# Kernel tuning notes

Hardware: AMD Instinct MI355X
Metric: run time of the kernel (lower is better)

The kernel has to match this reference:

```python
import jax, jax.numpy as jnp
import numpy as np

N_NODES = 50000
K_NEIGH = 32
D_IN = 128
D_OUT = 128
LEAKY_ALPHA = 0.2  # tf.nn.leaky_relu default


def setup_inputs() -> dict:
    key = jax.random.key(0)
    k1, k2, k3, k4 = jax.random.split(key, 4)
    glorot = lambda k, shape: jax.random.uniform(
        k, shape, jnp.float32, -1.0, 1.0) * np.sqrt(6.0 / (shape[0] + shape[1]))
    return {
        "self_vecs": jax.random.normal(k1, (N_NODES, D_IN), jnp.float32),
        "neigh_vecs": jax.random.normal(k2, (N_NODES * K_NEIGH, D_IN), jnp.float32),
        "feat_weights": glorot(k3, (D_IN, D_OUT)),
        "attn_weights": glorot(k4, (D_OUT, 1)),
        "bias": jnp.zeros((D_OUT,), jnp.float32),
        "num_neighbors": K_NEIGH,
    }


def reference(self_vecs, neigh_vecs, feat_weights, attn_weights, bias, num_neighbors):
    n = self_vecs.shape[0]
    from_neighs = neigh_vecs @ feat_weights            # [N*K, Dout]
    h_self = self_vecs @ feat_weights                  # [N, Dout]
    neigh_logits = (from_neighs @ attn_weights).reshape(n, num_neighbors)  # [N, K]
    self_logits = h_self @ attn_weights                # [N, 1]
    logits = neigh_logits + self_logits                # [N, K]
    coefs = jax.nn.softmax(jax.nn.leaky_relu(logits, LEAKY_ALPHA), axis=-1)
    # dropout rate = 0.0 -> identity
    h_neighs = jnp.einsum("nk,nkd->nd", coefs,
                          from_neighs.reshape(n, num_neighbors, -1))  # [N, Dout]
    return jax.nn.relu(h_self + h_neighs + bias)
```

## Files before the change

### kernel.cpp

```cpp
#include <hip/hip_runtime.h>


constexpr int D   = 128;
constexpr int KN  = 32;
constexpr int NPW = 4;
constexpr int LDP = 136;
constexpr int XR  = 33;
constexpr int XROWS_TOTAL = 4 * XR + 15;

typedef __bf16 bf16;
typedef __attribute__((ext_vector_type(8))) __bf16 bf16x8;
typedef __attribute__((ext_vector_type(4))) __bf16 bf16x4;
typedef __attribute__((ext_vector_type(4))) float  f32x4;

__global__ void prep_wt_kernel(const float* __restrict__ W, bf16* __restrict__ Wt) {
  int i = blockIdx.x * 256 + threadIdx.x;
  if (i < D * D) {
    int n = i >> 7, k = i & 127;
    Wt[i] = (bf16)W[(k << 7) + n];
  }
}

__global__ __launch_bounds__(256, 2)
void gat_kernel(const float* __restrict__ selfv,
                const float* __restrict__ neighv,
                const float* __restrict__ Wfp,
                const bf16*  __restrict__ Wt_g,
                const float* __restrict__ attn,
                const float* __restrict__ biasp,
                float* __restrict__ out,
                int nnodes, int use_ws)
{
  __shared__ __align__(16) bf16 Wt[D][LDP];
  __shared__ __align__(16) bf16 Xs[XROWS_TOTAL][LDP];

  const int tid  = threadIdx.x;
  const int w    = tid >> 6;
  const int lane = tid & 63;
  const int q    = lane >> 4;
  const int l15  = lane & 15;

  if (use_ws) {
    const ulonglong2* src = (const ulonglong2*)Wt_g;
    for (int i = tid; i < (D * D) / 8; i += 256) {
      int r = i >> 4, c8 = i & 15;
      *(ulonglong2*)&Wt[r][c8 << 3] = src[i];
    }
  } else {
    for (int i = tid; i < D * D; i += 256) {
      int n = i >> 7, k = i & 127;
      Wt[n][k] = (bf16)Wfp[(k << 7) + n];
    }
  }

  float av[8], bv[8];
  #pragma unroll
  for (int nt = 0; nt < 8; ++nt) {
    av[nt] = attn[nt * 16 + l15];
    bv[nt] = biasp[nt * 16 + l15];
  }

  __syncthreads();

  bf16* Xw = &Xs[w * XR][0];
  const float4* neigh4 = (const float4*)neighv;
  const float4* self4  = (const float4*)selfv;
  const int gw = blockIdx.x * 4 + w;

  for (int i = 0; i < NPW; ++i) {
    const int node = gw * NPW + i;
    if (node >= nnodes) break;

    {
      const size_t nb = (size_t)node * (KN * D / 4);
      const size_t sb = (size_t)node * (D / 4);
      #pragma unroll
      for (int it = 0; it < 17; ++it) {
        int idx = lane + it * 64;
        if (idx < 1056) {
          float4 v = (idx < 1024) ? neigh4[nb + idx] : self4[sb + (idx - 1024)];
          int row = idx >> 5, c4 = idx & 31;
          bf16x4 b = { (bf16)v.x, (bf16)v.y, (bf16)v.z, (bf16)v.w };
          *(bf16x4*)&Xw[row * LDP + (c4 << 2)] = b;
        }
      }
    }
    __threadfence_block();

    f32x4 acc[3][8];
    #pragma unroll
    for (int mt = 0; mt < 3; ++mt)
      #pragma unroll
      for (int nt = 0; nt < 8; ++nt)
        acc[mt][nt] = (f32x4){0.f, 0.f, 0.f, 0.f};

    #pragma unroll
    for (int ks = 0; ks < 4; ++ks) {
      bf16x8 A[3], B[8];
      #pragma unroll
      for (int mt = 0; mt < 3; ++mt)
        A[mt] = *(const bf16x8*)&Xw[(mt * 16 + l15) * LDP + ks * 32 + q * 8];
      #pragma unroll
      for (int nt = 0; nt < 8; ++nt)
        B[nt] = *(const bf16x8*)&Wt[nt * 16 + l15][ks * 32 + q * 8];
      #pragma unroll
      for (int mt = 0; mt < 3; ++mt)
        #pragma unroll
        for (int nt = 0; nt < 8; ++nt)
          acc[mt][nt] = __builtin_amdgcn_mfma_f32_16x16x32_bf16(A[mt], B[nt], acc[mt][nt], 0, 0, 0);
    }

    float lg[2][4];
    #pragma unroll
    for (int mt = 0; mt < 2; ++mt)
      #pragma unroll
      for (int r = 0; r < 4; ++r) {
        float v = 0.f;
        #pragma unroll
        for (int nt = 0; nt < 8; ++nt) v += acc[mt][nt][r] * av[nt];
        v += __shfl_xor(v, 1); v += __shfl_xor(v, 2);
        v += __shfl_xor(v, 4); v += __shfl_xor(v, 8);
        lg[mt][r] = v;
      }
    float sl;
    {
      float v = 0.f;
      #pragma unroll
      for (int nt = 0; nt < 8; ++nt) v += acc[2][nt][0] * av[nt];
      v += __shfl_xor(v, 1); v += __shfl_xor(v, 2);
      v += __shfl_xor(v, 4); v += __shfl_xor(v, 8);
      sl = __shfl(v, l15);
    }

    float e[2][4];
    float mx = -3.4e38f;
    #pragma unroll
    for (int mt = 0; mt < 2; ++mt)
      #pragma unroll
      for (int r = 0; r < 4; ++r) {
        float t = lg[mt][r] + sl;
        t = t > 0.f ? t : 0.2f * t;
        e[mt][r] = t;
        mx = fmaxf(mx, t);
      }
    mx = fmaxf(mx, __shfl_xor(mx, 16));
    mx = fmaxf(mx, __shfl_xor(mx, 32));
    float s = 0.f;
    #pragma unroll
    for (int mt = 0; mt < 2; ++mt)
      #pragma unroll
      for (int r = 0; r < 4; ++r) {
        e[mt][r] = __expf(e[mt][r] - mx);
        s += e[mt][r];
      }
    s += __shfl_xor(s, 16);
    s += __shfl_xor(s, 32);
    const float inv = 1.0f / s;

    #pragma unroll
    for (int nt = 0; nt < 8; ++nt) {
      float p = 0.f;
      #pragma unroll
      for (int mt = 0; mt < 2; ++mt)
        #pragma unroll
        for (int r = 0; r < 4; ++r)
          p += e[mt][r] * acc[mt][nt][r];
      p *= inv;
      p += __shfl_xor(p, 16);
      p += __shfl_xor(p, 32);
      float hs = __shfl(acc[2][nt][0], l15);
      float ov = fmaxf(hs + p + bv[nt], 0.f);
      if (q == (nt >> 1))
        out[(size_t)node * D + nt * 16 + l15] = ov;
    }
  }
}

extern "C" void kernel_launch(void* const* d_in, const int* in_sizes, int n_in,
                              void* d_out, int out_size, void* d_ws, size_t ws_size,
                              hipStream_t stream) {
  const float* selfv  = (const float*)d_in[0];
  const float* neighv = (const float*)d_in[1];
  const float* W      = (const float*)d_in[2];
  const float* attn   = (const float*)d_in[3];
  const float* biasp  = (const float*)d_in[4];
  float* out = (float*)d_out;
  const int nnodes = in_sizes[0] / D;

  const int use_ws = (ws_size >= (size_t)(D * D * sizeof(bf16))) ? 1 : 0;
  bf16* Wt_g = (bf16*)d_ws;
  if (use_ws)
    prep_wt_kernel<<<(D * D + 255) / 256, 256, 0, stream>>>(W, Wt_g);

  const int nwaves  = (nnodes + NPW - 1) / NPW;
  const int nblocks = (nwaves + 3) / 4;
  gat_kernel<<<nblocks, 256, 0, stream>>>(selfv, neighv, W, Wt_g, attn, biasp,
                                          out, nnodes, use_ws);
}
```

Baseline: 1.078 ms.

## Reassociate GAT: aggregate raw neighbours first, then project once per node

Folds the attention vector into the weights (W·a) so neighbour logits come from a 128-wide dot on raw inputs. The softmax-weighted sum runs over raw neighbour features plus the self vector, and a second pass applies the 128x128 projection once per node. The projection input is split into hi/lo bf16 parts to keep precision. This removes the per-neighbour 128x128 matmul in exchange for an extra kernel, an fp32 intermediate round-trip through the output buffer, and register-staged prefetch of the next node's neighbours.

After: 1.088 ms. No clear change (+0.9%).

```diff
diff --git a/kernel.cpp b/kernel.cpp
--- a/kernel.cpp
+++ b/kernel.cpp
@@ -3,175 +3,222 @@
 
 constexpr int D   = 128;
 constexpr int KN  = 32;
-constexpr int NPW = 4;
-constexpr int LDP = 136;
-constexpr int XR  = 33;
-constexpr int XROWS_TOTAL = 4 * XR + 15;
+constexpr int LDX = 136;
 
 typedef __bf16 bf16;
 typedef __attribute__((ext_vector_type(8))) __bf16 bf16x8;
-typedef __attribute__((ext_vector_type(4))) __bf16 bf16x4;
 typedef __attribute__((ext_vector_type(4))) float  f32x4;
 
-__global__ void prep_wt_kernel(const float* __restrict__ W, bf16* __restrict__ Wt) {
-  int i = blockIdx.x * 256 + threadIdx.x;
+__global__ void prep_kernel(const float* __restrict__ W,
+                            const float* __restrict__ attn,
+                            bf16* __restrict__ Wt,
+                            float* __restrict__ wa)
+{
+  const int i = blockIdx.x * 256 + threadIdx.x;
   if (i < D * D) {
-    int n = i >> 7, k = i & 127;
+    const int n = i >> 7, k = i & 127;
     Wt[i] = (bf16)W[(k << 7) + n];
   }
-}
-
-__global__ __launch_bounds__(256, 2)
-void gat_kernel(const float* __restrict__ selfv,
-                const float* __restrict__ neighv,
-                const float* __restrict__ Wfp,
-                const bf16*  __restrict__ Wt_g,
-                const float* __restrict__ attn,
-                const float* __restrict__ biasp,
-                float* __restrict__ out,
-                int nnodes, int use_ws)
+  if (i < D) {
+    float s = 0.f;
+    for (int n = 0; n < D; ++n) s += W[i * D + n] * attn[n];
+    wa[i] = s;
+  }
+}
+
+__global__ __launch_bounds__(64, 3)
+void gat_pass1(const float* __restrict__ selfv,
+               const float* __restrict__ neighv,
+               const float* __restrict__ Wfp,
+               const float* __restrict__ attnv,
+               const float* __restrict__ wa_g,
+               float* __restrict__ ybuf,
+               int nnodes, int npn, int use_ws)
 {
-  __shared__ __align__(16) bf16 Wt[D][LDP];
-  __shared__ __align__(16) bf16 Xs[XROWS_TOTAL][LDP];
-
-  const int tid  = threadIdx.x;
-  const int w    = tid >> 6;
-  const int lane = tid & 63;
-  const int q    = lane >> 4;
-  const int l15  = lane & 15;
-
+  __shared__ __align__(16) bf16 Xs[KN * LDX];
+  __shared__ __align__(16) bf16 wab[D];
+
+  const int lane = threadIdx.x;
+  const int q = lane >> 4, l15 = lane & 15;
+
+  float wa0, wa1;
   if (use_ws) {
-    const ulonglong2* src = (const ulonglong2*)Wt_g;
-    for (int i = tid; i < (D * D) / 8; i += 256) {
-      int r = i >> 4, c8 = i & 15;
-      *(ulonglong2*)&Wt[r][c8 << 3] = src[i];
-    }
+    float2 w2 = *(const float2*)&wa_g[2 * lane];
+    wa0 = w2.x; wa1 = w2.y;
   } else {
-    for (int i = tid; i < D * D; i += 256) {
-      int n = i >> 7, k = i & 127;
-      Wt[n][k] = (bf16)Wfp[(k << 7) + n];
-    }
-  }
-
-  float av[8], bv[8];
-  #pragma unroll
-  for (int nt = 0; nt < 8; ++nt) {
-    av[nt] = attn[nt * 16 + l15];
-    bv[nt] = biasp[nt * 16 + l15];
-  }
-
-  __syncthreads();
-
-  bf16* Xw = &Xs[w * XR][0];
+    float s0 = 0.f, s1 = 0.f;
+    for (int n = 0; n < D; ++n) {
+      const float an = attnv[n];
+      s0 += Wfp[(2 * lane) * D + n] * an;
+      s1 += Wfp[(2 * lane + 1) * D + n] * an;
+    }
+    wa0 = s0; wa1 = s1;
+  }
+  wab[2 * lane]     = (bf16)wa0;
+  wab[2 * lane + 1] = (bf16)wa1;
+
   const float4* neigh4 = (const float4*)neighv;
-  const float4* self4  = (const float4*)selfv;
-  const int gw = blockIdx.x * 4 + w;
-
-  for (int i = 0; i < NPW; ++i) {
-    const int node = gw * NPW + i;
+  const float2* self2  = (const float2*)selfv;
+  const int base = blockIdx.x * npn;
+  if (base >= nnodes) return;
+
+  float4 st[16];
+  float2 selfr;
+  {
+    const float4* p = neigh4 + (size_t)base * (KN * D / 4);
+    #pragma unroll
+    for (int c = 0; c < 8; ++c) {
+      st[2 * c]     = p[2 * (lane + 64 * c)];
+      st[2 * c + 1] = p[2 * (lane + 64 * c) + 1];
+    }
+    selfr = self2[(size_t)base * (D / 2) + lane];
+  }
+
+  for (int i = 0; i < npn; ++i) {
+    const int node = base + i;
     if (node >= nnodes) break;
 
-    {
-      const size_t nb = (size_t)node * (KN * D / 4);
-      const size_t sb = (size_t)node * (D / 4);
+    #pragma unroll
+    for (int c = 0; c < 8; ++c) {
+      const int cc = lane + 64 * c;
+      const int row = cc >> 4, c8 = cc & 15;
+      const float4 va = st[2 * c], vb = st[2 * c + 1];
+      bf16x8 b = { (bf16)va.x, (bf16)va.y, (bf16)va.z, (bf16)va.w,
+                   (bf16)vb.x, (bf16)vb.y, (bf16)vb.z, (bf16)vb.w };
+      *(bf16x8*)&Xs[row * LDX + c8 * 8] = b;
+    }
+    const float2 sv = selfr;
+
+    if (i + 1 < npn && node + 1 < nnodes) {
+      const float4* p = neigh4 + (size_t)(node + 1) * (KN * D / 4);
       #pragma unroll
-      for (int it = 0; it < 17; ++it) {
-        int idx = lane + it * 64;
-        if (idx < 1056) {
-          float4 v = (idx < 1024) ? neigh4[nb + idx] : self4[sb + (idx - 1024)];
-          int row = idx >> 5, c4 = idx & 31;
-          bf16x4 b = { (bf16)v.x, (bf16)v.y, (bf16)v.z, (bf16)v.w };
-          *(bf16x4*)&Xw[row * LDP + (c4 << 2)] = b;
-        }
+      for (int c = 0; c < 8; ++c) {
+        st[2 * c]     = p[2 * (lane + 64 * c)];
+        st[2 * c + 1] = p[2 * (lane + 64 * c) + 1];
       }
-    }
-    __threadfence_block();
-
-    f32x4 acc[3][8];
-    #pragma unroll
-    for (int mt = 0; mt < 3; ++mt)
-      #pragma unroll
-      for (int nt = 0; nt < 8; ++nt)
-        acc[mt][nt] = (f32x4){0.f, 0.f, 0.f, 0.f};
-
+      selfr = self2[(size_t)(node + 1) * (D / 2) + lane];
+    }
+
+    f32x4 acc0 = {0.f, 0.f, 0.f, 0.f}, acc1 = {0.f, 0.f, 0.f, 0.f};
     #pragma unroll
     for (int ks = 0; ks < 4; ++ks) {
-      bf16x8 A[3], B[8];
-      #pragma unroll
-      for (int mt = 0; mt < 3; ++mt)
-        A[mt] = *(const bf16x8*)&Xw[(mt * 16 + l15) * LDP + ks * 32 + q * 8];
-      #pragma unroll
-      for (int nt = 0; nt < 8; ++nt)
-        B[nt] = *(const bf16x8*)&Wt[nt * 16 + l15][ks * 32 + q * 8];
-      #pragma unroll
-      for (int mt = 0; mt < 3; ++mt)
-        #pragma unroll
-        for (int nt = 0; nt < 8; ++nt)
-          acc[mt][nt] = __builtin_amdgcn_mfma_f32_16x16x32_bf16(A[mt], B[nt], acc[mt][nt], 0, 0, 0);
-    }
-
-    float lg[2][4];
-    #pragma unroll
-    for (int mt = 0; mt < 2; ++mt)
-      #pragma unroll
-      for (int r = 0; r < 4; ++r) {
-        float v = 0.f;
-        #pragma unroll
-        for (int nt = 0; nt < 8; ++nt) v += acc[mt][nt][r] * av[nt];
-        v += __shfl_xor(v, 1); v += __shfl_xor(v, 2);
-        v += __shfl_xor(v, 4); v += __shfl_xor(v, 8);
-        lg[mt][r] = v;
-      }
-    float sl;
-    {
-      float v = 0.f;
-      #pragma unroll
-      for (int nt = 0; nt < 8; ++nt) v += acc[2][nt][0] * av[nt];
-      v += __shfl_xor(v, 1); v += __shfl_xor(v, 2);
-      v += __shfl_xor(v, 4); v += __shfl_xor(v, 8);
-      sl = __shfl(v, l15);
-    }
-
-    float e[2][4];
-    float mx = -3.4e38f;
-    #pragma unroll
-    for (int mt = 0; mt < 2; ++mt)
-      #pragma unroll
-      for (int r = 0; r < 4; ++r) {
-        float t = lg[mt][r] + sl;
-        t = t > 0.f ? t : 0.2f * t;
-        e[mt][r] = t;
-        mx = fmaxf(mx, t);
-      }
+      const bf16x8 B  = *(const bf16x8*)&wab[ks * 32 + q * 8];
+      const bf16x8 A0 = *(const bf16x8*)&Xs[l15 * LDX + ks * 32 + q * 8];
+      const bf16x8 A1 = *(const bf16x8*)&Xs[(16 + l15) * LDX + ks * 32 + q * 8];
+      acc0 = __builtin_amdgcn_mfma_f32_16x16x32_bf16(A0, B, acc0, 0, 0, 0);
+      acc1 = __builtin_amdgcn_mfma_f32_16x16x32_bf16(A1, B, acc1, 0, 0, 0);
+    }
+
+    float sl = sv.x * wa0 + sv.y * wa1;
+    sl += __shfl_xor(sl, 1);  sl += __shfl_xor(sl, 2);  sl += __shfl_xor(sl, 4);
+    sl += __shfl_xor(sl, 8);  sl += __shfl_xor(sl, 16); sl += __shfl_xor(sl, 32);
+
+    float e0[4], e1[4], mx = -3.4e38f;
+    #pragma unroll
+    for (int r = 0; r < 4; ++r) {
+      float t0 = acc0[r] + sl; t0 = t0 > 0.f ? t0 : 0.2f * t0;
+      float t1 = acc1[r] + sl; t1 = t1 > 0.f ? t1 : 0.2f * t1;
+      e0[r] = t0; e1[r] = t1;
+      mx = fmaxf(mx, fmaxf(t0, t1));
+    }
     mx = fmaxf(mx, __shfl_xor(mx, 16));
     mx = fmaxf(mx, __shfl_xor(mx, 32));
     float s = 0.f;
     #pragma unroll
-    for (int mt = 0; mt < 2; ++mt)
+    for (int r = 0; r < 4; ++r) {
+      e0[r] = __expf(e0[r] - mx); e1[r] = __expf(e1[r] - mx);
+      s += e0[r] + e1[r];
+    }
+    s += __shfl_xor(s, 16); s += __shfl_xor(s, 32);
+    const float inv = 1.0f / s;
+    #pragma unroll
+    for (int r = 0; r < 4; ++r) { e0[r] *= inv; e1[r] *= inv; }
+
+    float cf[32];
+    #pragma unroll
+    for (int k = 0; k < 32; ++k) {
+      const int src = ((k >> 2) & 3) * 16;
+      const float v = (k < 16) ? e0[k & 3] : e1[k & 3];
+      cf[k] = __int_as_float(__builtin_amdgcn_readlane(__float_as_int(v), src));
+    }
+
+    float z0 = 0.f, z1 = 0.f;
+    #pragma unroll
+    for (int r = 0; r < 32; ++r) {
+      const unsigned u = *(const unsigned*)&Xs[r * LDX + 2 * lane];
+      z0 += cf[r] * __uint_as_float(u << 16);
+      z1 += cf[r] * __uint_as_float(u & 0xffff0000u);
+    }
+    const float2 y = { sv.x + z0, sv.y + z1 };
+    *(float2*)&ybuf[(size_t)node * D + 2 * lane] = y;
+  }
+}
+
+__global__ __launch_bounds__(256, 2)
+void gat_pass2(const bf16* __restrict__ Wt_g,
+               const float* __restrict__ Wfp,
+               const float* __restrict__ biasp,
+               float* __restrict__ out,
+               int nnodes, int use_ws)
+{
+  const int tid = threadIdx.x, w = tid >> 6, lane = tid & 63;
+  const int q = lane >> 4, l15 = lane & 15;
+  const int t = blockIdx.x * 4 + w;
+  const int row0 = t * 16;
+  if (row0 >= nnodes) return;
+
+  float bv[8];
+  #pragma unroll
+  for (int nt = 0; nt < 8; ++nt) bv[nt] = biasp[nt * 16 + l15];
+
+  const int arow = row0 + l15;
+  const bool rv = arow < nnodes;
+
+  f32x4 acc[8];
+  #pragma unroll
+  for (int nt = 0; nt < 8; ++nt) acc[nt] = (f32x4){0.f, 0.f, 0.f, 0.f};
+
+  #pragma unroll
+  for (int ks = 0; ks < 4; ++ks) {
+    float a[8];
+    if (rv) {
+      const float4 v0 = *(const float4*)&out[(size_t)arow * D + ks * 32 + q * 8];
+      const float4 v1 = *(const float4*)&out[(size_t)arow * D + ks * 32 + q * 8 + 4];
+      a[0] = v0.x; a[1] = v0.y; a[2] = v0.z; a[3] = v0.w;
+      a[4] = v1.x; a[5] = v1.y; a[6] = v1.z; a[7] = v1.w;
+    } else {
       #pragma unroll
-      for (int r = 0; r < 4; ++r) {
-        e[mt][r] = __expf(e[mt][r] - mx);
-        s += e[mt][r];
+      for (int j = 0; j < 8; ++j) a[j] = 0.f;
+    }
+    bf16x8 Ah, Al;
+    #pragma unroll
+    for (int j = 0; j < 8; ++j) {
+      const bf16 h = (bf16)a[j];
+      Ah[j] = h;
+      Al[j] = (bf16)(a[j] - (float)h);
+    }
+    #pragma unroll
+    for (int nt = 0; nt < 8; ++nt) {
+      bf16x8 B;
+      if (use_ws) {
+        B = *(const bf16x8*)&Wt_g[(nt * 16 + l15) * D + ks * 32 + q * 8];
+      } else {
+        #pragma unroll
+        for (int j = 0; j < 8; ++j)
+          B[j] = (bf16)Wfp[(size_t)(ks * 32 + q * 8 + j) * D + nt * 16 + l15];
       }
-    s += __shfl_xor(s, 16);
-    s += __shfl_xor(s, 32);
-    const float inv = 1.0f / s;
-
-    #pragma unroll
-    for (int nt = 0; nt < 8; ++nt) {
-      float p = 0.f;
-      #pragma unroll
-      for (int mt = 0; mt < 2; ++mt)
-        #pragma unroll
-        for (int r = 0; r < 4; ++r)
-          p += e[mt][r] * acc[mt][nt][r];
-      p *= inv;
-      p += __shfl_xor(p, 16);
-      p += __shfl_xor(p, 32);
-      float hs = __shfl(acc[2][nt][0], l15);
-      float ov = fmaxf(hs + p + bv[nt], 0.f);
-      if (q == (nt >> 1))
-        out[(size_t)node * D + nt * 16 + l15] = ov;
+      acc[nt] = __builtin_amdgcn_mfma_f32_16x16x32_bf16(Ah, B, acc[nt], 0, 0, 0);
+      acc[nt] = __builtin_amdgcn_mfma_f32_16x16x32_bf16(Al, B, acc[nt], 0, 0, 0);
+    }
+  }
+
+  #pragma unroll
+  for (int nt = 0; nt < 8; ++nt) {
+    #pragma unroll
+    for (int r = 0; r < 4; ++r) {
+      const int row = row0 + q * 4 + r;
+      if (row < nnodes)
+        out[(size_t)row * D + nt * 16 + l15] = fmaxf(acc[nt][r] + bv[nt], 0.f);
     }
   }
 }
@@ -187,13 +234,19 @@
   float* out = (float*)d_out;
   const int nnodes = in_sizes[0] / D;
 
-  const int use_ws = (ws_size >= (size_t)(D * D * sizeof(bf16))) ? 1 : 0;
-  bf16* Wt_g = (bf16*)d_ws;
+  const size_t need = (size_t)D * D * sizeof(bf16) + D * sizeof(float);
+  const int use_ws = (ws_size >= need) ? 1 : 0;
+  bf16*  Wt_g = (bf16*)d_ws;
+  float* wa_g = (float*)((char*)d_ws + (size_t)D * D * sizeof(bf16));
   if (use_ws)
-    prep_wt_kernel<<<(D * D + 255) / 256, 256, 0, stream>>>(W, Wt_g);
-
-  const int nwaves  = (nnodes + NPW - 1) / NPW;
-  const int nblocks = (nwaves + 3) / 4;
-  gat_kernel<<<nblocks, 256, 0, stream>>>(selfv, neighv, W, Wt_g, attn, biasp,
-                                          out, nnodes, use_ws);
-}
+    prep_kernel<<<(D * D + 255) / 256, 256, 0, stream>>>(W, attn, Wt_g, wa_g);
+
+  const int nblk = 3072;
+  const int npn  = (nnodes + nblk - 1) / nblk;
+  gat_pass1<<<nblk, 64, 0, stream>>>(selfv, neighv, W, attn, wa_g, out,
+                                     nnodes, npn, use_ws);
+
+  const int ntiles = (nnodes + 15) / 16;
+  gat_pass2<<<(ntiles + 3) / 4, 256, 0, stream>>>(Wt_g, W, biasp, out,
+                                                  nnodes, use_ws);
+}
```
